# Performance work log

Measured on AMD Instinct MI355X. Metric: run time of the kernel, lower is better.

Reference implementation:

```python
import jax, jax.numpy as jnp
import numpy as np

D, K, STRIDE, PADDING = 5, 3, 1, 2
B, CIN, COUT, H, W = 32, 128, 256, 56, 56


def _conv(x, w, stride, padding):
    return jax.lax.conv_general_dilated(
        x, w, window_strides=(stride, stride),
        padding=[(padding, padding), (padding, padding)],
        dimension_numbers=("NCHW", "OIHW", "NCHW"))


def setup_inputs() -> dict:
    key = jax.random.key(0)
    k1, k2, k3 = jax.random.split(key, 3)
    x = jax.random.normal(k1, (B, CIN, H, W), dtype=jnp.float32)
    # kaiming-uniform-ish core init
    fan_in = CIN * K * K
    bound = float(np.sqrt(6.0 / fan_in))
    core = jax.random.uniform(k2, (COUT, CIN, K, K), dtype=jnp.float32,
                              minval=-bound, maxval=bound)
    periphery = jax.random.uniform(k3, (D * D - K * K,), dtype=jnp.float32,
                                   minval=-0.1, maxval=0.1)
    thresh = jnp.ones((COUT,), jnp.float32) * 0.1
    scale = jnp.array([10.0], jnp.float32)
    return {"x": x, "core": core, "periphery": periphery,
            "thresh": thresh, "scale": scale}


def reference(x, core, periphery, thresh, scale):
    pad = (D - K) // 2  # offset of the KxK core inside the DxD window
    # Dense core conv: embed KxK core at the center of a DxD kernel so core
    # and periphery share the same output grid (padding=PADDING for DxD).
    core_full = jnp.pad(core, ((0, 0), (0, 0), (pad, pad), (pad, pad)))
    core_out = _conv(x, core_full, STRIDE, PADDING)  # [B, COUT, Ho, Wo]

    # Periphery: one shared scalar per off-core offset, shared across all
    # in/out channels -> sum input over channels, conv with a 1x1-channel
    # DxD stencil whose core region is zero.
    periph_mask = np.ones((D, D), dtype=bool)
    periph_mask[pad:pad + K, pad:pad + K] = False
    periph_idx = np.flatnonzero(periph_mask)  # row-major off-core offsets
    pk = jnp.zeros((D * D,), x.dtype).at[periph_idx].set(periphery)
    pk = pk.reshape(1, 1, D, D)
    xs = jnp.sum(x, axis=1, keepdims=True)  # [B,1,H,W]
    periph_out = _conv(xs, pk, STRIDE, PADDING)  # [B,1,Ho,Wo]

    # Per-out-channel threshold/scale gating: periphery term is switched on
    # where the core response exceeds the channel threshold (soft gate).
    gate = jax.nn.sigmoid(scale[0] * (core_out - thresh[None, :, None, None]))
    return core_out + gate * periph_out
```

## Files before the change

kernel.cpp:

```cpp
#include <hip/hip_runtime.h>

typedef __attribute__((__ext_vector_type__(8))) _Float16 f16x8;
typedef __attribute__((__ext_vector_type__(4))) float f32x4;
typedef __attribute__((__ext_vector_type__(4))) int i32x4;

#define HW 56
#define HW2 3136
#define CIN 128
#define COUT 256
#define NB 32
#define NPIX 100352
#define PH 58

static __device__ __forceinline__ unsigned short f2h(float f) {
  _Float16 h = (_Float16)f;
  return __builtin_bit_cast(unsigned short, h);
}

#define GLD_LDS16(g, l)                                          \
  __builtin_amdgcn_global_load_lds(                              \
      (const __attribute__((address_space(1))) void*)(g),        \
      (__attribute__((address_space(3))) void*)(l), 16, 0, 0)

__global__ __launch_bounds__(256) void zero_halo(unsigned short* __restrict__ xp) {
  int t = blockIdx.x * 256 + threadIdx.x;
  int ck = t & 15;
  int pi = t >> 4;
  int b = pi / 228, r = pi - b * 228;
  int h, w;
  if (r < 58) { h = 0; w = r; }
  else if (r < 116) { h = 57; w = r - 58; }
  else { int q = r - 116; h = 1 + (q >> 1); w = (q & 1) * 57; }
  size_t off = (((size_t)(b * PH + h) * PH + w) << 8) + (ck << 4);
  *reinterpret_cast<i32x4*>((char*)xp + off) = (i32x4){0, 0, 0, 0};
}

__global__ __launch_bounds__(256) void prep_x(const float* __restrict__ x,
                                              unsigned short* __restrict__ xp,
                                              float* __restrict__ xs) {
  __shared__ float tile[CIN * 57];
  const int bh = blockIdx.x;
  const float* src = x + (size_t)(bh / HW) * CIN * HW2 + (size_t)(bh % HW) * HW;
  for (int idx = threadIdx.x; idx < CIN * HW; idx += 256) {
    int c = idx / HW, w = idx - c * HW;
    tile[c * 57 + w] = src[(size_t)c * HW2 + w];
  }
  __syncthreads();
  unsigned short* dst =
      xp + (((size_t)(bh / HW) * PH + (bh % HW) + 1) * PH + 1) * CIN;
  for (int idx = threadIdx.x; idx < HW * (CIN / 2); idx += 256) {
    int w = idx >> 6;
    int c = (idx & 63) << 1;
    unsigned lo = f2h(tile[c * 57 + w]);
    unsigned hi = f2h(tile[(c + 1) * 57 + w]);
    *reinterpret_cast<unsigned*>(&dst[w * CIN + c]) = lo | (hi << 16);
  }
  if (threadIdx.x < HW) {
    float s = 0.f;
    for (int c = 0; c < CIN; ++c) s += tile[c * 57 + threadIdx.x];
    xs[(size_t)bh * HW + threadIdx.x] = s;
  }
}

__global__ __launch_bounds__(256) void prep_w(const float* __restrict__ core,
                                              unsigned short* __restrict__ w_t) {
  int i = blockIdx.x * 256 + threadIdx.x;
  int c = i & 127;
  int p = (i >> 7) % 9;
  int m = i / (9 * 128);
  w_t[i] = f2h(core[(size_t)(m * CIN + c) * 9 + p]);
}

__global__ __launch_bounds__(256) void periph_k(const float* __restrict__ xs,
                                                const float* __restrict__ per,
                                                float* __restrict__ po) {
  int n = blockIdx.x * 256 + threadIdx.x;
  int b = n / HW2, r = n - b * HW2;
  int ho = r / HW, wo = r - ho * HW;
  const float* xb = xs + (size_t)b * HW2;
  const int pdy[16] = {0,0,0,0,0,1,1,2,2,3,3,4,4,4,4,4};
  const int pdx[16] = {0,1,2,3,4,0,4,0,4,0,4,0,1,2,3,4};
  float acc = 0.f;
#pragma unroll
  for (int t = 0; t < 16; ++t) {
    int h = ho + pdy[t] - 2, w = wo + pdx[t] - 2;
    if ((unsigned)h < HW && (unsigned)w < HW) acc += per[t] * xb[h * HW + w];
  }
  po[n] = acc;
}

__global__ __launch_bounds__(512, 2) void gemm_k(const unsigned short* __restrict__ xp,
                                                 const unsigned short* __restrict__ w_t,
                                                 const float* __restrict__ po,
                                                 const float* __restrict__ thresh,
                                                 const float* __restrict__ scale,
                                                 float* __restrict__ out) {
  __shared__ __align__(16) char sMem[2 * 49152];

  const int tid = threadIdx.x;
  const int lane = tid & 63;
  const int wid = tid >> 6;
  const int wm = wid >> 1;
  const int wn = wid & 1;

  const int bid = blockIdx.x;
  const int n0 = ((bid & 7) * 98 + (bid >> 3)) * 128;

  const int jr = lane >> 3;
  const int sw = ((lane & 7) ^ jr) << 4;
  const char* xpc = (const char*)xp;
  const char* wtc = (const char*)w_t;
  int aSrc[4], ldsA[4];
#pragma unroll
  for (int i = 0; i < 4; ++i) {
    int r = wid * 32 + i * 8 + jr;
    aSrc[i] = r * 9 * 256 + sw;
    ldsA[i] = (wid * 32 + i * 8) * 128;
  }
  int bSrc[2], ldsB[2];
#pragma unroll
  for (int i = 0; i < 2; ++i) {
    int r = wid * 16 + i * 8 + jr;
    int n = n0 + r;
    int b = n / HW2, rr = n - b * HW2;
    int h = rr / HW, w = rr - h * HW;
    bSrc[i] = ((b * PH + h + 1) * PH + (w + 1)) * 256 + sw;
    ldsB[i] = 32768 + (wid * 16 + i * 8) * 128;
  }

  int aro[4][2], bro[4][2];
#pragma unroll
  for (int i = 0; i < 4; ++i) {
#pragma unroll
    for (int ko = 0; ko < 2; ++ko) {
      int rowA = wm * 64 + i * 16 + (lane & 15);
      int rowB = wn * 64 + i * 16 + (lane & 15);
      int boc = ko * 64 + ((lane >> 4) << 4);
      aro[i][ko] = rowA * 128 + (boc ^ ((rowA & 7) << 4));
      bro[i][ko] = 32768 + rowB * 128 + (boc ^ ((rowB & 7) << 4));
    }
  }

  auto STAGE = [&](int buf, int step) {
    const int p = step >> 1;
    const int c0b = (step & 1) << 7;
    const int dy = p / 3 - 1, dx = p - (p / 3) * 3 - 1;
    const int offA = (p << 8) + c0b;
    const int offB = ((dy * PH + dx) << 8) + c0b;
    char* base = sMem + buf * 49152;
#pragma unroll
    for (int i = 0; i < 4; ++i) GLD_LDS16(wtc + aSrc[i] + offA, base + ldsA[i]);
#pragma unroll
    for (int i = 0; i < 2; ++i) GLD_LDS16(xpc + bSrc[i] + offB, base + ldsB[i]);
  };

  f32x4 acc[4][4] = {};

  STAGE(0, 0);
  __syncthreads();
  int cur = 0;
  for (int step = 0; step < 18; ++step) {
    if (step < 17) STAGE(cur ^ 1, step + 1);
    const char* base = sMem + cur * 49152;
#pragma unroll
    for (int ko = 0; ko < 2; ++ko) {
      f16x8 af[4], bfr[4];
#pragma unroll
      for (int i = 0; i < 4; ++i)
        af[i] = *reinterpret_cast<const f16x8*>(base + aro[i][ko]);
#pragma unroll
      for (int i = 0; i < 4; ++i)
        bfr[i] = *reinterpret_cast<const f16x8*>(base + bro[i][ko]);
      __builtin_amdgcn_s_setprio(1);
#pragma unroll
      for (int i = 0; i < 4; ++i)
#pragma unroll
        for (int j = 0; j < 4; ++j)
          acc[i][j] = __builtin_amdgcn_mfma_f32_16x16x32_f16(af[i], bfr[j], acc[i][j], 0, 0, 0);
      __builtin_amdgcn_s_setprio(0);
    }
    if (step < 17) {
      __syncthreads();
      cur ^= 1;
    }
  }

  const float sc = scale[0];
#pragma unroll
  for (int nj = 0; nj < 4; ++nj) {
    int n = n0 + wn * 64 + nj * 16 + (lane & 15);
    int b = n / HW2;
    int r = n - b * HW2;
    float pv = po[n];
    float* op = out + (size_t)b * (COUT * HW2) + r;
#pragma unroll
    for (int mi = 0; mi < 4; ++mi) {
      int cl = wm * 64 + mi * 16 + ((lane >> 4) << 2);
#pragma unroll
      for (int q = 0; q < 4; ++q) {
        float cv = acc[mi][nj][q];
        float g = 1.f / (1.f + __expf(-sc * (cv - thresh[cl + q])));
        op[(size_t)(cl + q) * HW2] = cv + g * pv;
      }
    }
  }
}

extern "C" void kernel_launch(void* const* d_in, const int* in_sizes, int n_in,
                              void* d_out, int out_size, void* d_ws, size_t ws_size,
                              hipStream_t stream) {
  (void)in_sizes; (void)n_in; (void)out_size; (void)ws_size;
  const float* x      = (const float*)d_in[0];
  const float* core   = (const float*)d_in[1];
  const float* per    = (const float*)d_in[2];
  const float* thresh = (const float*)d_in[3];
  const float* scale  = (const float*)d_in[4];
  float* out = (float*)d_out;

  char* ws = (char*)d_ws;
  unsigned short* xp  = (unsigned short*)ws;
  unsigned short* w_t = (unsigned short*)(ws + 27557888);
  float* xs           = (float*)(ws + 28147712);
  float* po           = (float*)(ws + 28549120);

  zero_halo<<<(NB * 228 * 16) / 256, 256, 0, stream>>>(xp);
  prep_x<<<NB * HW, 256, 0, stream>>>(x, xp, xs);
  prep_w<<<(COUT * 9 * CIN) / 256, 256, 0, stream>>>(core, w_t);
  periph_k<<<NPIX / 256, 256, 0, stream>>>(xs, per, po);
  gemm_k<<<NPIX / 128, 512, 0, stream>>>(xp, w_t, po, thresh, scale, out);
}
```

Before: 128.2 us.

## Enlarge GEMM tile to 256x256 with raw barriers and partial vmcnt waits

The implicit-GEMM conv kernel's output tile grows from 256 channels x 128 pixels to 256 x 256 pixels per block. Each warp now computes 128x64, which halves the weight reloads per pixel and doubles MFMA work per staged byte. The pipeline swaps __syncthreads for explicit s_barrier plus s_waitcnt vmcnt, so the next stage's loads stay in flight while the current stage is consumed. Thresholds are cached in LDS. The cost is more accumulator registers (128 floats per lane) and 129KB of LDS, so only one block fits per CU. The grid also halves to 392 blocks, which reduces occupancy and wave-level parallelism.

```diff
diff --git a/kernel.cpp b/kernel.cpp
--- a/kernel.cpp
+++ b/kernel.cpp
@@ -95,51 +95,54 @@
                                                  const float* __restrict__ thresh,
                                                  const float* __restrict__ scale,
                                                  float* __restrict__ out) {
-  __shared__ __align__(16) char sMem[2 * 49152];
+  __shared__ __align__(16) char sMem[2 * 65536 + 1024];
 
   const int tid = threadIdx.x;
   const int lane = tid & 63;
   const int wid = tid >> 6;
-  const int wm = wid >> 1;
-  const int wn = wid & 1;
+  const int wm = wid >> 2;
+  const int wn = wid & 3;
 
   const int bid = blockIdx.x;
-  const int n0 = ((bid & 7) * 98 + (bid >> 3)) * 128;
-
-  const int jr = lane >> 3;
-  const int sw = ((lane & 7) ^ jr) << 4;
+  const int n0 = ((bid & 7) * 49 + (bid >> 3)) << 8;
+
+  float* sTh = (float*)(sMem + 131072);
+  if (tid < 256) sTh[tid] = thresh[tid];
+
+  const int slot = tid & 7;
+  const int trow = tid >> 3;
+  const int sw = (slot ^ (trow & 7)) << 4;
   const char* xpc = (const char*)xp;
   const char* wtc = (const char*)w_t;
-  int aSrc[4], ldsA[4];
-#pragma unroll
-  for (int i = 0; i < 4; ++i) {
-    int r = wid * 32 + i * 8 + jr;
-    aSrc[i] = r * 9 * 256 + sw;
-    ldsA[i] = (wid * 32 + i * 8) * 128;
-  }
-  int bSrc[2], ldsB[2];
-#pragma unroll
-  for (int i = 0; i < 2; ++i) {
-    int r = wid * 16 + i * 8 + jr;
-    int n = n0 + r;
+  int aOff[4], bOff[4];
+#pragma unroll
+  for (int q = 0; q < 4; ++q) {
+    int row = q * 64 + trow;
+    aOff[q] = row * (9 * 256) + sw;
+    int n = n0 + row;
     int b = n / HW2, rr = n - b * HW2;
     int h = rr / HW, w = rr - h * HW;
-    bSrc[i] = ((b * PH + h + 1) * PH + (w + 1)) * 256 + sw;
-    ldsB[i] = 32768 + (wid * 16 + i * 8) * 128;
-  }
-
-  int aro[4][2], bro[4][2];
-#pragma unroll
-  for (int i = 0; i < 4; ++i) {
+    bOff[q] = ((b * PH + h + 1) * PH + (w + 1)) * 256 + sw;
+  }
+  const int ldsw = wid * 1024;
+
+  int aro[8][2], bro[4][2];
+#pragma unroll
+  for (int i = 0; i < 8; ++i)
 #pragma unroll
     for (int ko = 0; ko < 2; ++ko) {
-      int rowA = wm * 64 + i * 16 + (lane & 15);
-      int rowB = wn * 64 + i * 16 + (lane & 15);
+      int rowA = wm * 128 + i * 16 + (lane & 15);
       int boc = ko * 64 + ((lane >> 4) << 4);
       aro[i][ko] = rowA * 128 + (boc ^ ((rowA & 7) << 4));
-      bro[i][ko] = 32768 + rowB * 128 + (boc ^ ((rowB & 7) << 4));
-    }
-  }
+    }
+#pragma unroll
+  for (int j = 0; j < 4; ++j)
+#pragma unroll
+    for (int ko = 0; ko < 2; ++ko) {
+      int rowB = wn * 64 + j * 16 + (lane & 15);
+      int boc = ko * 64 + ((lane >> 4) << 4);
+      bro[j][ko] = 32768 + rowB * 128 + (boc ^ ((rowB & 7) << 4));
+    }
 
   auto STAGE = [&](int buf, int step) {
     const int p = step >> 1;
@@ -147,59 +150,66 @@
     const int dy = p / 3 - 1, dx = p - (p / 3) * 3 - 1;
     const int offA = (p << 8) + c0b;
     const int offB = ((dy * PH + dx) << 8) + c0b;
-    char* base = sMem + buf * 49152;
-#pragma unroll
-    for (int i = 0; i < 4; ++i) GLD_LDS16(wtc + aSrc[i] + offA, base + ldsA[i]);
-#pragma unroll
-    for (int i = 0; i < 2; ++i) GLD_LDS16(xpc + bSrc[i] + offB, base + ldsB[i]);
+    char* base = sMem + buf * 65536;
+#pragma unroll
+    for (int q = 0; q < 4; ++q)
+      GLD_LDS16(wtc + aOff[q] + offA, base + ldsw + q * 8192);
+#pragma unroll
+    for (int q = 0; q < 4; ++q)
+      GLD_LDS16(xpc + bOff[q] + offB, base + 32768 + ldsw + q * 8192);
   };
 
-  f32x4 acc[4][4] = {};
+  f32x4 acc[8][4] = {};
 
   STAGE(0, 0);
   __syncthreads();
-  int cur = 0;
-  for (int step = 0; step < 18; ++step) {
-    if (step < 17) STAGE(cur ^ 1, step + 1);
-    const char* base = sMem + cur * 49152;
-#pragma unroll
-    for (int ko = 0; ko < 2; ++ko) {
-      f16x8 af[4], bfr[4];
-#pragma unroll
-      for (int i = 0; i < 4; ++i)
-        af[i] = *reinterpret_cast<const f16x8*>(base + aro[i][ko]);
-#pragma unroll
-      for (int i = 0; i < 4; ++i)
-        bfr[i] = *reinterpret_cast<const f16x8*>(base + bro[i][ko]);
+
+#pragma unroll
+  for (int s = 0; s < 18; ++s) {
+    const char* base = sMem + (s & 1) * 65536;
+    __builtin_amdgcn_s_barrier();
+    if (s < 17) {
+      STAGE((s + 1) & 1, s + 1);
+      asm volatile("s_waitcnt vmcnt(8)" ::: "memory");
+    } else {
+      asm volatile("s_waitcnt vmcnt(0)" ::: "memory");
+    }
+    __builtin_amdgcn_s_barrier();
+    f16x8 bfr[4][2];
+#pragma unroll
+    for (int j = 0; j < 4; ++j)
+#pragma unroll
+      for (int ko = 0; ko < 2; ++ko)
+        bfr[j][ko] = *reinterpret_cast<const f16x8*>(base + bro[j][ko]);
+#pragma unroll
+    for (int i = 0; i < 8; ++i) {
+      f16x8 a0 = *reinterpret_cast<const f16x8*>(base + aro[i][0]);
+      f16x8 a1 = *reinterpret_cast<const f16x8*>(base + aro[i][1]);
       __builtin_amdgcn_s_setprio(1);
 #pragma unroll
-      for (int i = 0; i < 4; ++i)
-#pragma unroll
-        for (int j = 0; j < 4; ++j)
-          acc[i][j] = __builtin_amdgcn_mfma_f32_16x16x32_f16(af[i], bfr[j], acc[i][j], 0, 0, 0);
+      for (int j = 0; j < 4; ++j) {
+        acc[i][j] = __builtin_amdgcn_mfma_f32_16x16x32_f16(a0, bfr[j][0], acc[i][j], 0, 0, 0);
+        acc[i][j] = __builtin_amdgcn_mfma_f32_16x16x32_f16(a1, bfr[j][1], acc[i][j], 0, 0, 0);
+      }
       __builtin_amdgcn_s_setprio(0);
     }
-    if (step < 17) {
-      __syncthreads();
-      cur ^= 1;
-    }
   }
 
   const float sc = scale[0];
 #pragma unroll
-  for (int nj = 0; nj < 4; ++nj) {
-    int n = n0 + wn * 64 + nj * 16 + (lane & 15);
+  for (int j = 0; j < 4; ++j) {
+    int n = n0 + wn * 64 + j * 16 + (lane & 15);
     int b = n / HW2;
     int r = n - b * HW2;
     float pv = po[n];
     float* op = out + (size_t)b * (COUT * HW2) + r;
 #pragma unroll
-    for (int mi = 0; mi < 4; ++mi) {
-      int cl = wm * 64 + mi * 16 + ((lane >> 4) << 2);
+    for (int i = 0; i < 8; ++i) {
+      int cl = wm * 128 + i * 16 + ((lane >> 4) << 2);
 #pragma unroll
       for (int q = 0; q < 4; ++q) {
-        float cv = acc[mi][nj][q];
-        float g = 1.f / (1.f + __expf(-sc * (cv - thresh[cl + q])));
+        float cv = acc[i][j][q];
+        float g = 1.f / (1.f + __expf(-sc * (cv - sTh[cl + q])));
         op[(size_t)(cl + q) * HW2] = cv + g * pv;
       }
     }
@@ -227,5 +237,5 @@
   prep_x<<<NB * HW, 256, 0, stream>>>(x, xp, xs);
   prep_w<<<(COUT * 9 * CIN) / 256, 256, 0, stream>>>(core, w_t);
   periph_k<<<NPIX / 256, 256, 0, stream>>>(xs, per, po);
-  gemm_k<<<NPIX / 128, 512, 0, stream>>>(xp, w_t, po, thresh, scale, out);
-}
+  gemm_k<<<NPIX / 256, 512, 0, stream>>>(xp, w_t, po, thresh, scale, out);
+}
```

Result: faster. 120.5 us (-6.1%).

## Halve GEMM K-step to 32 channels, shrink LDS, and use split barriers

Applied to the files above, without the earlier changes.

The conv GEMM now stages 32 input channels per step (36 steps instead of 18), so each LDS buffer shrinks from 48KB to 24KB and launch bounds ask for 4 blocks per CU instead of 2. The loop swaps __syncthreads for raw s_barrier with an explicit vmcnt wait, and the LDS swizzle is reworked for the 64-byte rows. The aim is more resident waves to hide load latency. The cost is twice as many barriers and fewer MFMAs between them, with register pressure possibly limiting occupancy anyway. Threshold values are also loaded as one vector instead of scalar reads.

```diff
diff --git a/kernel.cpp b/kernel.cpp
--- a/kernel.cpp
+++ b/kernel.cpp
@@ -89,13 +89,13 @@
   po[n] = acc;
 }
 
-__global__ __launch_bounds__(512, 2) void gemm_k(const unsigned short* __restrict__ xp,
+__global__ __launch_bounds__(512, 4) void gemm_k(const unsigned short* __restrict__ xp,
                                                  const unsigned short* __restrict__ w_t,
                                                  const float* __restrict__ po,
                                                  const float* __restrict__ thresh,
                                                  const float* __restrict__ scale,
                                                  float* __restrict__ out) {
-  __shared__ __align__(16) char sMem[2 * 49152];
+  __shared__ __align__(16) char sMem[2 * 24576];
 
   const int tid = threadIdx.x;
   const int lane = tid & 63;
@@ -104,102 +104,100 @@
   const int wn = wid & 1;
 
   const int bid = blockIdx.x;
-  const int n0 = ((bid & 7) * 98 + (bid >> 3)) * 128;
-
-  const int jr = lane >> 3;
-  const int sw = ((lane & 7) ^ jr) << 4;
+  const int n0 = ((bid & 7) * 98 + (bid >> 3)) << 7;
+
+  const int l4 = lane >> 2;
+  const int ls = lane & 3;
   const char* xpc = (const char*)xp;
   const char* wtc = (const char*)w_t;
-  int aSrc[4], ldsA[4];
-#pragma unroll
-  for (int i = 0; i < 4; ++i) {
-    int r = wid * 32 + i * 8 + jr;
-    aSrc[i] = r * 9 * 256 + sw;
-    ldsA[i] = (wid * 32 + i * 8) * 128;
-  }
-  int bSrc[2], ldsB[2];
-#pragma unroll
-  for (int i = 0; i < 2; ++i) {
-    int r = wid * 16 + i * 8 + jr;
+  int aSrc[2];
+#pragma unroll
+  for (int k = 0; k < 2; ++k) {
+    int r = wid * 32 + k * 16 + l4;
+    aSrc[k] = r * 2304 + ((ls ^ ((r >> 1) & 3)) << 4);
+  }
+  const int aDst0 = wid * 2048;
+  int bSrc;
+  {
+    int r = wid * 16 + l4;
     int n = n0 + r;
     int b = n / HW2, rr = n - b * HW2;
     int h = rr / HW, w = rr - h * HW;
-    bSrc[i] = ((b * PH + h + 1) * PH + (w + 1)) * 256 + sw;
-    ldsB[i] = 32768 + (wid * 16 + i * 8) * 128;
-  }
-
-  int aro[4][2], bro[4][2];
+    bSrc = ((b * PH + h + 1) * PH + (w + 1)) * 256 + ((ls ^ ((r >> 1) & 3)) << 4);
+  }
+  const int bDst = 16384 + wid * 1024;
+
+  int aro[4], bro[4];
 #pragma unroll
   for (int i = 0; i < 4; ++i) {
-#pragma unroll
-    for (int ko = 0; ko < 2; ++ko) {
-      int rowA = wm * 64 + i * 16 + (lane & 15);
-      int rowB = wn * 64 + i * 16 + (lane & 15);
-      int boc = ko * 64 + ((lane >> 4) << 4);
-      aro[i][ko] = rowA * 128 + (boc ^ ((rowA & 7) << 4));
-      bro[i][ko] = 32768 + rowB * 128 + (boc ^ ((rowB & 7) << 4));
-    }
-  }
-
-  auto STAGE = [&](int buf, int step) {
-    const int p = step >> 1;
-    const int c0b = (step & 1) << 7;
+    int rowA = wm * 64 + i * 16 + (lane & 15);
+    aro[i] = rowA * 64 + ((((lane >> 4) ^ (rowA >> 1)) & 3) << 4);
+  }
+#pragma unroll
+  for (int j = 0; j < 4; ++j) {
+    int rowB = wn * 64 + j * 16 + (lane & 15);
+    bro[j] = 16384 + rowB * 64 + ((((lane >> 4) ^ (rowB >> 1)) & 3) << 4);
+  }
+
+  auto STAGE = [&](int buf, int t) {
+    const int p = t >> 2;
+    const int cq = t & 3;
     const int dy = p / 3 - 1, dx = p - (p / 3) * 3 - 1;
-    const int offA = (p << 8) + c0b;
-    const int offB = ((dy * PH + dx) << 8) + c0b;
-    char* base = sMem + buf * 49152;
-#pragma unroll
-    for (int i = 0; i < 4; ++i) GLD_LDS16(wtc + aSrc[i] + offA, base + ldsA[i]);
-#pragma unroll
-    for (int i = 0; i < 2; ++i) GLD_LDS16(xpc + bSrc[i] + offB, base + ldsB[i]);
+    const int offA = (p << 8) + (cq << 6);
+    const int offB = ((dy * PH + dx) << 8) + (cq << 6);
+    char* base = sMem + buf * 24576;
+    GLD_LDS16(wtc + aSrc[0] + offA, base + aDst0);
+    GLD_LDS16(wtc + aSrc[1] + offA, base + aDst0 + 1024);
+    GLD_LDS16(xpc + bSrc + offB, base + bDst);
   };
 
   f32x4 acc[4][4] = {};
 
   STAGE(0, 0);
   __syncthreads();
-  int cur = 0;
-  for (int step = 0; step < 18; ++step) {
-    if (step < 17) STAGE(cur ^ 1, step + 1);
-    const char* base = sMem + cur * 49152;
-#pragma unroll
-    for (int ko = 0; ko < 2; ++ko) {
-      f16x8 af[4], bfr[4];
-#pragma unroll
-      for (int i = 0; i < 4; ++i)
-        af[i] = *reinterpret_cast<const f16x8*>(base + aro[i][ko]);
-#pragma unroll
-      for (int i = 0; i < 4; ++i)
-        bfr[i] = *reinterpret_cast<const f16x8*>(base + bro[i][ko]);
+
+  for (int t = 0; t < 36; ++t) {
+    const char* base = sMem + (t & 1) * 24576;
+    __builtin_amdgcn_s_barrier();
+    if (t < 35) {
+      STAGE((t + 1) & 1, t + 1);
+      asm volatile("s_waitcnt vmcnt(3)" ::: "memory");
+    } else {
+      asm volatile("s_waitcnt vmcnt(0)" ::: "memory");
+    }
+    __builtin_amdgcn_s_barrier();
+
+    f16x8 bfr[4];
+#pragma unroll
+    for (int j = 0; j < 4; ++j)
+      bfr[j] = *reinterpret_cast<const f16x8*>(base + bro[j]);
+#pragma unroll
+    for (int i = 0; i < 4; ++i) {
+      f16x8 af = *reinterpret_cast<const f16x8*>(base + aro[i]);
       __builtin_amdgcn_s_setprio(1);
 #pragma unroll
-      for (int i = 0; i < 4; ++i)
-#pragma unroll
-        for (int j = 0; j < 4; ++j)
-          acc[i][j] = __builtin_amdgcn_mfma_f32_16x16x32_f16(af[i], bfr[j], acc[i][j], 0, 0, 0);
+      for (int j = 0; j < 4; ++j)
+        acc[i][j] = __builtin_amdgcn_mfma_f32_16x16x32_f16(af, bfr[j], acc[i][j], 0, 0, 0);
       __builtin_amdgcn_s_setprio(0);
     }
-    if (step < 17) {
-      __syncthreads();
-      cur ^= 1;
-    }
   }
 
   const float sc = scale[0];
 #pragma unroll
-  for (int nj = 0; nj < 4; ++nj) {
-    int n = n0 + wn * 64 + nj * 16 + (lane & 15);
+  for (int j = 0; j < 4; ++j) {
+    int n = n0 + wn * 64 + j * 16 + (lane & 15);
     int b = n / HW2;
     int r = n - b * HW2;
     float pv = po[n];
     float* op = out + (size_t)b * (COUT * HW2) + r;
 #pragma unroll
-    for (int mi = 0; mi < 4; ++mi) {
-      int cl = wm * 64 + mi * 16 + ((lane >> 4) << 2);
+    for (int i = 0; i < 4; ++i) {
+      int cl = wm * 64 + i * 16 + ((lane >> 4) << 2);
+      f32x4 th = *reinterpret_cast<const f32x4*>(&thresh[cl]);
 #pragma unroll
       for (int q = 0; q < 4; ++q) {
-        float cv = acc[mi][nj][q];
-        float g = 1.f / (1.f + __expf(-sc * (cv - thresh[cl + q])));
+        float cv = acc[i][j][q];
+        float g = 1.f / (1.f + __expf(-sc * (cv - th[q])));
         op[(size_t)(cl + q) * HW2] = cv + g * pv;
       }
     }
```

Measured after the change: 124.3 us. -3.1%, faster.
